# Kernel tuning notes

Hardware: AMD Instinct MI355X
Metric: run time of the kernel (lower is better)

Reference implementation:

```python
import jax, jax.numpy as jnp
import numpy as np

N, E, G = 100000, 1600000, 2048
F_NODE, F_EDGE, H, T = 32, 8, 128, 12


def _lin(key, fan_in, fan_out):
    k1, k2 = jax.random.split(key)
    s = 1.0 / np.sqrt(fan_in)
    W = jax.random.uniform(k1, (fan_in, fan_out), jnp.float32, -s, s)
    b = jax.random.uniform(k2, (fan_out,), jnp.float32, -s, s)
    return W, b


def setup_inputs() -> dict:
    key = jax.random.key(0)
    ks = jax.random.split(key, 12)
    x = jax.random.normal(ks[0], (N, F_NODE), jnp.float32)
    edge_index = jax.random.randint(ks[1], (2, E), 0, N, jnp.int64)
    edge_attr = jax.random.normal(ks[2], (E, F_EDGE), jnp.float32)
    batch = jnp.sort(jax.random.randint(ks[3], (N,), 0, G, jnp.int64))
    We1, be1 = _lin(ks[4], F_EDGE, F_NODE)   # conv1 edge lin: edge_dim -> in_channels
    W1a, b1a = _lin(ks[5], F_NODE, H)
    W1b, b1b = _lin(ks[6], H, H)
    We2, be2 = _lin(ks[7], F_EDGE, H)        # conv2 edge lin: edge_dim -> hidden
    W2a, b2a = _lin(ks[8], H, H)
    W2b, b2b = _lin(ks[9], H, H)
    Wl1, bl1 = _lin(ks[10], H, H)
    Wl2, bl2 = _lin(ks[11], H, T)
    return dict(x=x, edge_index=edge_index, edge_attr=edge_attr, batch=batch,
                We1=We1, be1=be1, W1a=W1a, b1a=b1a, W1b=W1b, b1b=b1b,
                We2=We2, be2=be2, W2a=W2a, b2a=b2a, W2b=W2b, b2b=b2b,
                Wl1=Wl1, bl1=bl1, Wl2=Wl2, bl2=bl2)


def _gine_conv(x, src, dst, edge_attr, We, be, Wa, ba, Wb, bb):
    # message: relu(x_j + Lin(edge_attr)), scatter-add to target, then MLP on (1+eps)*x + agg (eps=0)
    m = jax.nn.relu(x[src] + edge_attr @ We + be)          # [E, C]
    agg = jax.ops.segment_sum(m, dst, num_segments=x.shape[0])
    h = x + agg
    return jax.nn.elu(h @ Wa + ba) @ Wb + bb


def reference(x, edge_index, edge_attr, batch,
              We1, be1, W1a, b1a, W1b, b1b,
              We2, be2, W2a, b2a, W2b, b2b,
              Wl1, bl1, Wl2, bl2):
    src, dst = edge_index[0], edge_index[1]
    h = _gine_conv(x, src, dst, edge_attr, We1, be1, W1a, b1a, W1b, b1b)
    h = jax.nn.elu(h)  # dropout is identity at eval
    h = _gine_conv(h, src, dst, edge_attr, We2, be2, W2a, b2a, W2b, b2b)
    h = jax.nn.elu(h)
    hg = jax.ops.segment_sum(h, batch, num_segments=G)     # global add pool [G, H]
    hg = jax.nn.relu(hg @ Wl1 + bl1)
    return hg @ Wl2 + bl2                                  # [G, T]
```

## Files before the change

kernel.cpp:

```cpp
#include <hip/hip_runtime.h>
#include <math.h>

#define F_NODE 32
#define F_EDGE 8
#define HID 128
#define CAPB 6144

typedef __attribute__((ext_vector_type(2))) _Float16 f16x2;
typedef __attribute__((ext_vector_type(8))) _Float16 f16x8;
typedef __attribute__((ext_vector_type(4))) float f32x4;

__device__ __forceinline__ float elu_f(float x) { return x > 0.f ? x : expf(x) - 1.f; }

__device__ __forceinline__ unsigned h2u(f16x2 h) { union { f16x2 h; unsigned u; } x; x.h = h; return x.u; }
__device__ __forceinline__ f16x2 u2h(unsigned u) { union { unsigned u; f16x2 h; } x; x.u = u; return x.h; }
__device__ __forceinline__ unsigned packh2(float lo, float hi) {
    f16x2 v; v.x = (_Float16)lo; v.y = (_Float16)hi; return h2u(v);
}
__device__ __forceinline__ unsigned short f2h_bits(float f) {
    _Float16 h = (_Float16)f; union { _Float16 h; unsigned short u; } x; x.h = h; return x.u;
}
__device__ __forceinline__ f16x8 frag_from(uint4 v) { union { uint4 u; f16x8 f; } x; x.u = v; return x.f; }
__device__ __forceinline__ f16x2 duph(f16x8 v, int k) { f16x2 d; d.x = v[k]; d.y = v[k]; return d; }

__global__ void prep_kernel(const float* __restrict__ x, const float* __restrict__ ea,
                            const int* __restrict__ dst,
                            unsigned* __restrict__ xh, unsigned* __restrict__ eab,
                            const float* __restrict__ W1a, const float* __restrict__ W1b,
                            const float* __restrict__ W2a, const float* __restrict__ W2b,
                            const float* __restrict__ Wl1, const float* __restrict__ Wl2,
                            uint4* __restrict__ P1a, uint4* __restrict__ P1b,
                            uint4* __restrict__ P2a, uint4* __restrict__ P2b,
                            uint4* __restrict__ P3a, uint4* __restrict__ P3b,
                            int* __restrict__ cnt, int nx, int ne2, int E)
{
    int i = blockIdx.x * 256 + threadIdx.x;
    if (i < nx) {
        float2 v = ((const float2*)x)[i];
        xh[i] = packh2(v.x, v.y);
        return;
    }
    i -= nx;
    if (i < ne2) {
        float2 v = ((const float2*)ea)[i];
        eab[i] = packh2(v.x, v.y);
        return;
    }
    i -= ne2;
    if (i < 8960) {
        int f = i;
        if (f >= 8704) {
            f -= 8704;
            int lane = f & 63;
            int ks = f >> 6;
            int col = lane & 15;
            int k0 = ks * 32 + (lane >> 4) * 8;
            float w[8];
#pragma unroll
            for (int j = 0; j < 8; ++j) w[j] = col < 12 ? Wl2[(size_t)(k0 + j) * 12 + col] : 0.f;
            uint4 v;
            v.x = packh2(w[0], w[1]);
            v.y = packh2(w[2], w[3]);
            v.z = packh2(w[4], w[5]);
            v.w = packh2(w[6], w[7]);
            P3b[f] = v;
            return;
        }
        const float* W; uint4* P; int KS;
        if (f < 512)       { W = W1a; P = P1a; KS = 1; }
        else if (f < 2560) { W = W1b; P = P1b; KS = 4; f -= 512; }
        else if (f < 4608) { W = W2a; P = P2a; KS = 4; f -= 2560; }
        else if (f < 6656) { W = W2b; P = P2b; KS = 4; f -= 4608; }
        else               { W = Wl1; P = P3a; KS = 4; f -= 6656; }
        int lane = f & 63;
        int rem = f >> 6;
        int ks = rem % KS, ct = rem / KS;
        int col = ct * 16 + (lane & 15);
        int k0 = ks * 32 + (lane >> 4) * 8;
        float w[8];
#pragma unroll
        for (int j = 0; j < 8; ++j) w[j] = W[(size_t)(k0 + j) * HID + col];
        uint4 v;
        v.x = packh2(w[0], w[1]);
        v.y = packh2(w[2], w[3]);
        v.z = packh2(w[4], w[5]);
        v.w = packh2(w[6], w[7]);
        P[f] = v;
        return;
    }
    i -= 8960;
    if (i < E) atomicAdd(&cnt[dst[i]], 1);
}

__global__ void scan1_kernel(const int* __restrict__ in, int* __restrict__ out,
                             int* __restrict__ part, int n) {
    __shared__ int s[256];
    int t = threadIdx.x;
    int base = blockIdx.x * 1024 + t * 4;
    int v0 = base + 0 < n ? in[base + 0] : 0;
    int v1 = base + 1 < n ? in[base + 1] : 0;
    int v2 = base + 2 < n ? in[base + 2] : 0;
    int v3 = base + 3 < n ? in[base + 3] : 0;
    int tot = v0 + v1 + v2 + v3;
    s[t] = tot;
    __syncthreads();
    for (int off = 1; off < 256; off <<= 1) {
        int val = (t >= off) ? s[t - off] : 0;
        __syncthreads();
        s[t] += val;
        __syncthreads();
    }
    int pre = s[t] - tot;
    if (base + 0 < n) out[base + 0] = pre;
    if (base + 1 < n) out[base + 1] = pre + v0;
    if (base + 2 < n) out[base + 2] = pre + v0 + v1;
    if (base + 3 < n) out[base + 3] = pre + v0 + v1 + v2;
    if (t == 255) part[blockIdx.x] = s[255];
}

__global__ void scan2_kernel(int* part, int nb) {
    __shared__ int s[256];
    int t = threadIdx.x;
    int v = t < nb ? part[t] : 0;
    s[t] = v;
    __syncthreads();
    for (int off = 1; off < 256; off <<= 1) {
        int val = (t >= off) ? s[t - off] : 0;
        __syncthreads();
        s[t] += val;
        __syncthreads();
    }
    if (t < nb) part[t] = s[t] - v;
}

__global__ void scan3_kernel(int* __restrict__ out, const int* __restrict__ part,
                             int* __restrict__ curB, int* __restrict__ curFine,
                             int n, int total) {
    int i = blockIdx.x * blockDim.x + threadIdx.x;
    if (i < n) {
        int v = out[i] + part[i >> 10];
        out[i] = v;
        curFine[i] = v;
        if ((i & 255) == 0) curB[i >> 8] = v;
    }
    if (i == 0) out[n] = total;
}

__global__ __launch_bounds__(256) void binA_kernel(
    const int* __restrict__ dst, const int* __restrict__ src,
    int* __restrict__ curB, int2* __restrict__ tmp, int E, int NB)
{
    __shared__ int hist[512];
    __shared__ int basev[512];
    const int tid = threadIdx.x;
    const int base = blockIdx.x * 4096;
    for (int i = tid; i < NB; i += 256) hist[i] = 0;
    __syncthreads();
    int d[16];
#pragma unroll
    for (int k = 0; k < 16; ++k) {
        int e = base + k * 256 + tid;
        d[k] = (e < E) ? dst[e] : -1;
        if (d[k] >= 0) atomicAdd(&hist[d[k] >> 8], 1);
    }
    __syncthreads();
    for (int i = tid; i < NB; i += 256) {
        int c = hist[i];
        basev[i] = c > 0 ? atomicAdd(&curB[i], c) : 0;
        hist[i] = 0;
    }
    __syncthreads();
#pragma unroll
    for (int k = 0; k < 16; ++k) {
        int e = base + k * 256 + tid;
        if (d[k] >= 0) {
            int b = d[k] >> 8;
            int r = atomicAdd(&hist[b], 1);
            tmp[basev[b] + r] = make_int2(e | ((d[k] & 255) << 22), src[e]);
        }
    }
}

__global__ __launch_bounds__(256) void binB_kernel(
    const int2* __restrict__ tmp, const int* __restrict__ off,
    int* __restrict__ curFine, int2* __restrict__ pair, int N)
{
    __shared__ int ldsCur[256];
    __shared__ int2 stage[CAPB];
    const int b = blockIdx.x;
    const int tid = threadIdx.x;
    const int node0 = b << 8;
    const int nend = min(node0 + 256, N);
    const int base = off[node0];
    const int end = off[nend];
    const int S = end - base;
    if (S <= CAPB) {
        int node = node0 + tid;
        ldsCur[tid] = (node < nend ? off[node] : end) - base;
        __syncthreads();
        for (int j = tid; j < S; j += 256) {
            int2 rec = tmp[base + j];
            int dloc = ((unsigned)rec.x) >> 22;
            int slot = atomicAdd(&ldsCur[dloc], 1);
            stage[slot] = make_int2(rec.x & 0x3FFFFF, rec.y);
        }
        __syncthreads();
        for (int j = tid; j < S; j += 256)
            pair[base + j] = stage[j];
    } else {
        for (int j = tid; j < S; j += 256) {
            int2 rec = tmp[base + j];
            int dloc = ((unsigned)rec.x) >> 22;
            int pos = atomicAdd(&curFine[node0 + dloc], 1);
            pair[pos] = make_int2(rec.x & 0x3FFFFF, rec.y);
        }
    }
}

__global__ __launch_bounds__(256) void agg1_kernel(
    const float* __restrict__ x, const unsigned* __restrict__ xh,
    const uint4* __restrict__ eab4,
    const float* __restrict__ We, const float* __restrict__ be,
    const int* __restrict__ off, const int2* __restrict__ pair,
    unsigned* __restrict__ aggh, int N)
{
    int wave = (blockIdx.x * 256 + threadIdx.x) >> 6;
    if (wave >= N) return;
    int lane = threadIdx.x & 63;
    int fp = lane & 15, eg = lane >> 4;
    int j0 = fp * 2;
    f16x2 w2[F_EDGE];
#pragma unroll
    for (int k = 0; k < F_EDGE; ++k)
        w2[k] = u2h(packh2(We[k * F_NODE + j0], We[k * F_NODE + j0 + 1]));
    f16x2 bias2 = u2h(packh2(be[j0], be[j0 + 1]));
    f16x2 zero2 = u2h(0u);
    int i0 = __builtin_amdgcn_readfirstlane(off[wave]);
    int i1 = __builtin_amdgcn_readfirstlane(off[wave + 1]);
    float acc0 = 0.f, acc1 = 0.f;
    for (int i = i0; i < i1; i += 4) {
        int ii = i + eg;
        if (ii < i1) {
            int2 p = pair[ii];
            f16x8 ev = frag_from(eab4[p.x]);
            f16x2 m = bias2 + u2h(xh[(size_t)p.y * 16 + fp]);
#pragma unroll
            for (int k = 0; k < F_EDGE; ++k)
                m = duph(ev, k) * w2[k] + m;
            m = __builtin_elementwise_max(m, zero2);
            acc0 += (float)m.x;
            acc1 += (float)m.y;
        }
    }
    acc0 += __shfl_xor(acc0, 16, 64);
    acc0 += __shfl_xor(acc0, 32, 64);
    acc1 += __shfl_xor(acc1, 16, 64);
    acc1 += __shfl_xor(acc1, 32, 64);
    if (eg == 0) {
        float2 xo = *(const float2*)&x[(size_t)wave * F_NODE + j0];
        aggh[(size_t)wave * 16 + fp] = packh2(xo.x + acc0, xo.y + acc1);
    }
}

__global__ __launch_bounds__(256) void agg2_kernel(
    const unsigned* __restrict__ hh,
    const uint4* __restrict__ eab4,
    const float* __restrict__ We, const float* __restrict__ be,
    const int* __restrict__ off, const int2* __restrict__ pair,
    unsigned* __restrict__ aggh, int N)
{
    int wave = (blockIdx.x * 256 + threadIdx.x) >> 6;
    if (wave >= N) return;
    int lane = threadIdx.x & 63;
    int j0 = lane * 2;
    f16x2 w2[F_EDGE];
#pragma unroll
    for (int k = 0; k < F_EDGE; ++k)
        w2[k] = u2h(packh2(We[k * HID + j0], We[k * HID + j0 + 1]));
    f16x2 bias2 = u2h(packh2(be[j0], be[j0 + 1]));
    f16x2 zero2 = u2h(0u);
    int i0 = __builtin_amdgcn_readfirstlane(off[wave]);
    int i1 = __builtin_amdgcn_readfirstlane(off[wave + 1]);
    float acc0 = 0.f, acc1 = 0.f;
    int i = i0;
    for (; i + 7 < i1; i += 8) {
        int2 p[8];
        unsigned u[8];
        f16x8 ev[8];
#pragma unroll
        for (int k = 0; k < 8; ++k) p[k] = pair[i + k];
#pragma unroll
        for (int k = 0; k < 8; ++k) u[k] = hh[(size_t)p[k].y * 64 + lane];
#pragma unroll
        for (int k = 0; k < 8; ++k) ev[k] = frag_from(eab4[p[k].x]);
        f16x2 m[8];
#pragma unroll
        for (int k = 0; k < 8; ++k) m[k] = bias2 + u2h(u[k]);
#pragma unroll
        for (int kk = 0; kk < F_EDGE; ++kk) {
#pragma unroll
            for (int k = 0; k < 8; ++k)
                m[k] = duph(ev[k], kk) * w2[kk] + m[k];
        }
        f16x2 s = __builtin_elementwise_max(m[0], zero2);
#pragma unroll
        for (int k = 1; k < 8; ++k) s = s + __builtin_elementwise_max(m[k], zero2);
        acc0 += (float)s.x;
        acc1 += (float)s.y;
    }
    for (; i < i1; ++i) {
        int2 p0 = pair[i];
        f16x8 e0 = frag_from(eab4[p0.x]);
        f16x2 m0 = bias2 + u2h(hh[(size_t)p0.y * 64 + lane]);
#pragma unroll
        for (int k = 0; k < F_EDGE; ++k)
            m0 = duph(e0, k) * w2[k] + m0;
        m0 = __builtin_elementwise_max(m0, zero2);
        acc0 += (float)m0.x;
        acc1 += (float)m0.y;
    }
    f16x2 self = u2h(hh[(size_t)wave * 64 + lane]);
    aggh[(size_t)wave * 64 + lane] = packh2((float)self.x + acc0, (float)self.y + acc1);
}

__device__ __forceinline__ void put_tile_elu_h(unsigned short* t, f32x4 v, int rbase, int c, int stride) {
#pragma unroll
    for (int j = 0; j < 4; ++j)
        t[(rbase + j) * stride + c] = f2h_bits(elu_f(v[j]));
}
__device__ __forceinline__ void put_tile_relu_h(unsigned short* t, f32x4 v, int rbase, int c, int stride) {
#pragma unroll
    for (int j = 0; j < 4; ++j)
        t[(rbase + j) * stride + c] = f2h_bits(fmaxf(v[j], 0.f));
}

template <int K, bool POOL>
__global__ __launch_bounds__(256) void mlp_mfma_kernel(
    const uint4* __restrict__ inb,
    const uint4* __restrict__ WaP, const float* __restrict__ ba,
    const uint4* __restrict__ WbP, const float* __restrict__ bb,
    uint4* __restrict__ outb,
    const int* __restrict__ batch, float* __restrict__ hg,
    int nrows)
{
    constexpr int KS_A = K / 32;
    constexpr int SA = K + 8;
    constexpr int ST = HID + 8;
    constexpr int STF = HID + 4;
    __shared__ __align__(16) unsigned short a_s[32 * SA];
    __shared__ __align__(16) unsigned short t_s[32 * ST];
    __shared__ float p_s[POOL ? 32 * STF : 1];
    __shared__ int batch_s[POOL ? 32 : 1];

    const int tid = threadIdx.x;
    const int row0 = blockIdx.x * 32;

    constexpr int Q = K / 8;
    for (int idx = tid; idx < 32 * Q; idx += 256) {
        int r = idx / Q, q = idx % Q;
        uint4 v = make_uint4(0, 0, 0, 0);
        if (row0 + r < nrows) v = inb[(size_t)(row0 + r) * Q + q];
        *(uint4*)&a_s[r * SA + q * 8] = v;
    }
    if (POOL && tid < 32)
        batch_s[tid] = (row0 + tid < nrows) ? batch[row0 + tid] : -1;
    __syncthreads();

    const int lane = tid & 63;
    const int w = tid >> 6;
    const int rb = w >> 1;
    const int cg = (w & 1) * 4;
    const int cf = lane & 15;
    const int g = lane >> 4;
    const int arow = rb * 16 + cf;

    f32x4 acc0, acc1, acc2, acc3;
    {
        float c0 = ba[(cg + 0) * 16 + cf], c1 = ba[(cg + 1) * 16 + cf];
        float c2 = ba[(cg + 2) * 16 + cf], c3 = ba[(cg + 3) * 16 + cf];
        acc0 = (f32x4){c0, c0, c0, c0};
        acc1 = (f32x4){c1, c1, c1, c1};
        acc2 = (f32x4){c2, c2, c2, c2};
        acc3 = (f32x4){c3, c3, c3, c3};
    }
#pragma unroll
    for (int ks = 0; ks < KS_A; ++ks) {
        f16x8 a = *(const f16x8*)&a_s[arow * SA + ks * 32 + g * 8];
        acc0 = __builtin_amdgcn_mfma_f32_16x16x32_f16(a, frag_from(WaP[((cg + 0) * KS_A + ks) * 64 + lane]), acc0, 0, 0, 0);
        acc1 = __builtin_amdgcn_mfma_f32_16x16x32_f16(a, frag_from(WaP[((cg + 1) * KS_A + ks) * 64 + lane]), acc1, 0, 0, 0);
        acc2 = __builtin_amdgcn_mfma_f32_16x16x32_f16(a, frag_from(WaP[((cg + 2) * KS_A + ks) * 64 + lane]), acc2, 0, 0, 0);
        acc3 = __builtin_amdgcn_mfma_f32_16x16x32_f16(a, frag_from(WaP[((cg + 3) * KS_A + ks) * 64 + lane]), acc3, 0, 0, 0);
    }
    {
        int rbase = rb * 16 + g * 4;
        put_tile_elu_h(t_s, acc0, rbase, (cg + 0) * 16 + cf, ST);
        put_tile_elu_h(t_s, acc1, rbase, (cg + 1) * 16 + cf, ST);
        put_tile_elu_h(t_s, acc2, rbase, (cg + 2) * 16 + cf, ST);
        put_tile_elu_h(t_s, acc3, rbase, (cg + 3) * 16 + cf, ST);
    }
    __syncthreads();

    {
        float c0 = bb[(cg + 0) * 16 + cf], c1 = bb[(cg + 1) * 16 + cf];
        float c2 = bb[(cg + 2) * 16 + cf], c3 = bb[(cg + 3) * 16 + cf];
        acc0 = (f32x4){c0, c0, c0, c0};
        acc1 = (f32x4){c1, c1, c1, c1};
        acc2 = (f32x4){c2, c2, c2, c2};
        acc3 = (f32x4){c3, c3, c3, c3};
    }
#pragma unroll
    for (int ks = 0; ks < 4; ++ks) {
        f16x8 a = *(const f16x8*)&t_s[arow * ST + ks * 32 + g * 8];
        acc0 = __builtin_amdgcn_mfma_f32_16x16x32_f16(a, frag_from(WbP[((cg + 0) * 4 + ks) * 64 + lane]), acc0, 0, 0, 0);
        acc1 = __builtin_amdgcn_mfma_f32_16x16x32_f16(a, frag_from(WbP[((cg + 1) * 4 + ks) * 64 + lane]), acc1, 0, 0, 0);
        acc2 = __builtin_amdgcn_mfma_f32_16x16x32_f16(a, frag_from(WbP[((cg + 2) * 4 + ks) * 64 + lane]), acc2, 0, 0, 0);
        acc3 = __builtin_amdgcn_mfma_f32_16x16x32_f16(a, frag_from(WbP[((cg + 3) * 4 + ks) * 64 + lane]), acc3, 0, 0, 0);
    }

    if (POOL) {
        int rbase = rb * 16 + g * 4;
#pragma unroll
        for (int j = 0; j < 4; ++j) {
            p_s[(rbase + j) * STF + (cg + 0) * 16 + cf] = elu_f(acc0[j]);
            p_s[(rbase + j) * STF + (cg + 1) * 16 + cf] = elu_f(acc1[j]);
            p_s[(rbase + j) * STF + (cg + 2) * 16 + cf] = elu_f(acc2[j]);
            p_s[(rbase + j) * STF + (cg + 3) * 16 + cf] = elu_f(acc3[j]);
        }
        __syncthreads();
        int f = tid & 127, grp = tid >> 7;
        float acc = 0.f;
        int cur = -1;
#pragma unroll 4
        for (int r = 0; r < 16; ++r) {
            int rr = grp * 16 + r;
            int b = batch_s[rr];
            if (b >= 0) {
                if (b != cur) {
                    if (cur >= 0) atomicAdd(&hg[(size_t)cur * HID + f], acc);
                    acc = 0.f;
                    cur = b;
                }
                acc += p_s[rr * STF + f];
            }
        }
        if (cur >= 0) atomicAdd(&hg[(size_t)cur * HID + f], acc);
    } else {
        __syncthreads();
        int rbase = rb * 16 + g * 4;
        put_tile_elu_h(t_s, acc0, rbase, (cg + 0) * 16 + cf, ST);
        put_tile_elu_h(t_s, acc1, rbase, (cg + 1) * 16 + cf, ST);
        put_tile_elu_h(t_s, acc2, rbase, (cg + 2) * 16 + cf, ST);
        put_tile_elu_h(t_s, acc3, rbase, (cg + 3) * 16 + cf, ST);
        __syncthreads();
        for (int idx = tid; idx < 32 * 16; idx += 256) {
            int r = idx >> 4, q = idx & 15;
            if (row0 + r < nrows)
                outb[(size_t)(row0 + r) * 16 + q] = *(const uint4*)&t_s[r * ST + q * 8];
        }
    }
}

__global__ __launch_bounds__(256) void head_mfma_kernel(
    const float* __restrict__ hg,
    const uint4* __restrict__ Wl1P, const float* __restrict__ bl1,
    const uint4* __restrict__ Wl2P, const float* __restrict__ bl2,
    float* __restrict__ out, int G)
{
    constexpr int ST = HID + 8;
    __shared__ __align__(16) unsigned short a_s[32 * ST];
    __shared__ __align__(16) unsigned short t_s[32 * ST];

    const int tid = threadIdx.x;
    const int row0 = blockIdx.x * 32;

    for (int idx = tid; idx < 32 * HID; idx += 256) {
        int r = idx >> 7, c = idx & 127;
        float v = (row0 + r < G) ? hg[(size_t)(row0 + r) * HID + c] : 0.f;
        a_s[r * ST + c] = f2h_bits(v);
    }
    __syncthreads();

    const int lane = tid & 63;
    const int w = tid >> 6;
    const int rb = w >> 1;
    const int cg = (w & 1) * 4;
    const int cf = lane & 15;
    const int g = lane >> 4;
    const int arow = rb * 16 + cf;

    f32x4 acc0, acc1, acc2, acc3;
    {
        float c0 = bl1[(cg + 0) * 16 + cf], c1 = bl1[(cg + 1) * 16 + cf];
        float c2 = bl1[(cg + 2) * 16 + cf], c3 = bl1[(cg + 3) * 16 + cf];
        acc0 = (f32x4){c0, c0, c0, c0};
        acc1 = (f32x4){c1, c1, c1, c1};
        acc2 = (f32x4){c2, c2, c2, c2};
        acc3 = (f32x4){c3, c3, c3, c3};
    }
#pragma unroll
    for (int ks = 0; ks < 4; ++ks) {
        f16x8 a = *(const f16x8*)&a_s[arow * ST + ks * 32 + g * 8];
        acc0 = __builtin_amdgcn_mfma_f32_16x16x32_f16(a, frag_from(Wl1P[((cg + 0) * 4 + ks) * 64 + lane]), acc0, 0, 0, 0);
        acc1 = __builtin_amdgcn_mfma_f32_16x16x32_f16(a, frag_from(Wl1P[((cg + 1) * 4 + ks) * 64 + lane]), acc1, 0, 0, 0);
        acc2 = __builtin_amdgcn_mfma_f32_16x16x32_f16(a, frag_from(Wl1P[((cg + 2) * 4 + ks) * 64 + lane]), acc2, 0, 0, 0);
        acc3 = __builtin_amdgcn_mfma_f32_16x16x32_f16(a, frag_from(Wl1P[((cg + 3) * 4 + ks) * 64 + lane]), acc3, 0, 0, 0);
    }
    {
        int rbase = rb * 16 + g * 4;
        put_tile_relu_h(t_s, acc0, rbase, (cg + 0) * 16 + cf, ST);
        put_tile_relu_h(t_s, acc1, rbase, (cg + 1) * 16 + cf, ST);
        put_tile_relu_h(t_s, acc2, rbase, (cg + 2) * 16 + cf, ST);
        put_tile_relu_h(t_s, acc3, rbase, (cg + 3) * 16 + cf, ST);
    }
    __syncthreads();

    if ((w & 1) == 0) {
        float c0 = cf < 12 ? bl2[cf] : 0.f;
        f32x4 acc = (f32x4){c0, c0, c0, c0};
#pragma unroll
        for (int ks = 0; ks < 4; ++ks) {
            f16x8 a = *(const f16x8*)&t_s[arow * ST + ks * 32 + g * 8];
            acc = __builtin_amdgcn_mfma_f32_16x16x32_f16(a, frag_from(Wl2P[ks * 64 + lane]), acc, 0, 0, 0);
        }
        if (cf < 12) {
            int rbase = rb * 16 + g * 4;
#pragma unroll
            for (int j = 0; j < 4; ++j) {
                int row = row0 + rbase + j;
                if (row < G) out[(size_t)row * 12 + cf] = acc[j];
            }
        }
    }
}

extern "C" void kernel_launch(void* const* d_in, const int* in_sizes, int n_in,
                              void* d_out, int out_size, void* d_ws, size_t ws_size,
                              hipStream_t stream)
{
    const float* x    = (const float*)d_in[0];
    const int*   ei   = (const int*)d_in[1];
    const float* ea   = (const float*)d_in[2];
    const int*   batch = (const int*)d_in[3];
    const float* We1 = (const float*)d_in[4];
    const float* be1 = (const float*)d_in[5];
    const float* W1a = (const float*)d_in[6];
    const float* b1a = (const float*)d_in[7];
    const float* W1b = (const float*)d_in[8];
    const float* b1b = (const float*)d_in[9];
    const float* We2 = (const float*)d_in[10];
    const float* be2 = (const float*)d_in[11];
    const float* W2a = (const float*)d_in[12];
    const float* b2a = (const float*)d_in[13];
    const float* W2b = (const float*)d_in[14];
    const float* b2b = (const float*)d_in[15];
    const float* Wl1 = (const float*)d_in[16];
    const float* bl1 = (const float*)d_in[17];
    const float* Wl2 = (const float*)d_in[18];
    const float* bl2 = (const float*)d_in[19];
    float* out = (float*)d_out;

    const int N = in_sizes[0] / F_NODE;
    const int E = in_sizes[1] / 2;
    const int G = out_size / 12;
    const int NB = (N + 255) >> 8;

    const int* srcp = ei;
    const int* dstp = ei + E;

    char* wsb = (char*)d_ws;
    auto alloc = [&](size_t bytes) -> char* {
        char* p = wsb;
        wsb += (bytes + 15) & ~(size_t)15;
        return p;
    };
    int* cnt     = (int*)alloc((size_t)N * 4);
    int* off     = (int*)alloc((size_t)(N + 1) * 4);
    int* part    = (int*)alloc(256 * 4);
    int* curB    = (int*)alloc(512 * 4);
    int* curFine = (int*)alloc((size_t)N * 4);
    int2* tmp    = (int2*)alloc((size_t)E * 8);
    int2* pair   = (int2*)alloc((size_t)E * 8);
    unsigned* xh   = (unsigned*)alloc((size_t)N * 16 * 4);
    unsigned* eab  = (unsigned*)alloc((size_t)E * 4 * 4);
    unsigned* agg1h = (unsigned*)alloc((size_t)N * 16 * 4);
    unsigned* h1h   = (unsigned*)alloc((size_t)N * 64 * 4);
    unsigned* agg2h = (unsigned*)alloc((size_t)N * 64 * 4);
    float* hg  = (float*)alloc((size_t)G * HID * 4);
    uint4* P1a = (uint4*)alloc(512 * 16);
    uint4* P1b = (uint4*)alloc(2048 * 16);
    uint4* P2a = (uint4*)alloc(2048 * 16);
    uint4* P2b = (uint4*)alloc(2048 * 16);
    uint4* P3a = (uint4*)alloc(2048 * 16);
    uint4* P3b = (uint4*)alloc(256 * 16);

    (void)hipMemsetAsync(cnt, 0, (size_t)N * sizeof(int), stream);
    (void)hipMemsetAsync(hg, 0, (size_t)G * HID * sizeof(float), stream);

    {
        int nx = N * 16, ne2 = E * 4;
        long long total = (long long)nx + ne2 + 8960 + E;
        hipLaunchKernelGGL(prep_kernel, dim3((unsigned)((total + 255) / 256)), dim3(256), 0, stream,
                           x, ea, dstp, xh, eab, W1a, W1b, W2a, W2b, Wl1, Wl2,
                           P1a, P1b, P2a, P2b, P3a, P3b, cnt, nx, ne2, E);
    }
    int nscan = (N + 1023) / 1024;
    hipLaunchKernelGGL(scan1_kernel, dim3(nscan), dim3(256), 0, stream, cnt, off, part, N);
    hipLaunchKernelGGL(scan2_kernel, dim3(1), dim3(256), 0, stream, part, nscan);
    hipLaunchKernelGGL(scan3_kernel, dim3((N + 255) / 256), dim3(256), 0, stream,
                       off, part, curB, curFine, N, E);
    hipLaunchKernelGGL(binA_kernel, dim3((E + 4095) / 4096), dim3(256), 0, stream,
                       dstp, srcp, curB, tmp, E, NB);
    hipLaunchKernelGGL(binB_kernel, dim3(NB), dim3(256), 0, stream,
                       tmp, off, curFine, pair, N);

    hipLaunchKernelGGL(agg1_kernel, dim3((N + 3) / 4), dim3(256), 0, stream,
                       x, xh, (const uint4*)eab, We1, be1, off, pair, agg1h, N);
    hipLaunchKernelGGL((mlp_mfma_kernel<F_NODE, false>), dim3((N + 31) / 32), dim3(256), 0, stream,
                       (const uint4*)agg1h, P1a, b1a, P1b, b1b, (uint4*)h1h,
                       (const int*)nullptr, (float*)nullptr, N);

    hipLaunchKernelGGL(agg2_kernel, dim3((N + 3) / 4), dim3(256), 0, stream,
                       h1h, (const uint4*)eab, We2, be2, off, pair, agg2h, N);
    hipLaunchKernelGGL((mlp_mfma_kernel<HID, true>), dim3((N + 31) / 32), dim3(256), 0, stream,
                       (const uint4*)agg2h, P2a, b2a, P2b, b2b, (uint4*)nullptr,
                       batch, hg, N);

    hipLaunchKernelGGL(head_mfma_kernel, dim3((G + 31) / 32), dim3(256), 0, stream,
                       hg, P3a, bl1, P3b, bl2, out, G);
}
```

Before: 375.3 us.

## Pre-sort edge attributes by destination and gather FP8 hidden features in conv2

binB now writes a source array plus a copy of each edge's attribute vector in destination-sorted order. Both aggregation kernels can then stream edge features contiguously instead of gathering them by edge id. The first MLP also writes an FP8 copy of the hidden features, which agg2 gathers at half the bytes per neighbor compared with FP16. This cuts random-access traffic in the dominant gather at the cost of lower precision for layer-2 messages, an extra sorted-copy write, and buffer aliasing (h8 reuses tmp, agg2h reuses eab).

After: 368.5 us. No clear change (-1.8%).

```diff
diff --git a/kernel.cpp b/kernel.cpp
--- a/kernel.cpp
+++ b/kernel.cpp
@@ -9,6 +9,7 @@
 typedef __attribute__((ext_vector_type(2))) _Float16 f16x2;
 typedef __attribute__((ext_vector_type(8))) _Float16 f16x8;
 typedef __attribute__((ext_vector_type(4))) float f32x4;
+typedef __attribute__((ext_vector_type(2))) float f32x2;
 
 __device__ __forceinline__ float elu_f(float x) { return x > 0.f ? x : expf(x) - 1.f; }
 
@@ -19,6 +20,9 @@
 }
 __device__ __forceinline__ unsigned short f2h_bits(float f) {
     _Float16 h = (_Float16)f; union { _Float16 h; unsigned short u; } x; x.h = h; return x.u;
+}
+__device__ __forceinline__ float hbits2f(unsigned short b) {
+    union { unsigned short u; _Float16 h; } x; x.u = b; return (float)x.h;
 }
 __device__ __forceinline__ f16x8 frag_from(uint4 v) { union { uint4 u; f16x8 f; } x; x.u = v; return x.f; }
 __device__ __forceinline__ f16x2 duph(f16x8 v, int k) { f16x2 d; d.x = v[k]; d.y = v[k]; return d; }
@@ -183,7 +187,8 @@
 
 __global__ __launch_bounds__(256) void binB_kernel(
     const int2* __restrict__ tmp, const int* __restrict__ off,
-    int* __restrict__ curFine, int2* __restrict__ pair, int N)
+    int* __restrict__ curFine, const uint4* __restrict__ eab4,
+    int* __restrict__ srcarr, uint4* __restrict__ easrt, int N)
 {
     __shared__ int ldsCur[256];
     __shared__ int2 stage[CAPB];
@@ -205,23 +210,28 @@
             stage[slot] = make_int2(rec.x & 0x3FFFFF, rec.y);
         }
         __syncthreads();
-        for (int j = tid; j < S; j += 256)
-            pair[base + j] = stage[j];
+        for (int j = tid; j < S; j += 256) {
+            int2 rec = stage[j];
+            srcarr[base + j] = rec.y;
+            easrt[base + j] = eab4[rec.x];
+        }
     } else {
         for (int j = tid; j < S; j += 256) {
             int2 rec = tmp[base + j];
             int dloc = ((unsigned)rec.x) >> 22;
+            int e = rec.x & 0x3FFFFF;
             int pos = atomicAdd(&curFine[node0 + dloc], 1);
-            pair[pos] = make_int2(rec.x & 0x3FFFFF, rec.y);
+            srcarr[pos] = rec.y;
+            easrt[pos] = eab4[e];
         }
     }
 }
 
 __global__ __launch_bounds__(256) void agg1_kernel(
     const float* __restrict__ x, const unsigned* __restrict__ xh,
-    const uint4* __restrict__ eab4,
+    const uint4* __restrict__ easrt,
     const float* __restrict__ We, const float* __restrict__ be,
-    const int* __restrict__ off, const int2* __restrict__ pair,
+    const int* __restrict__ off, const int* __restrict__ srcarr,
     unsigned* __restrict__ aggh, int N)
 {
     int wave = (blockIdx.x * 256 + threadIdx.x) >> 6;
@@ -241,9 +251,9 @@
     for (int i = i0; i < i1; i += 4) {
         int ii = i + eg;
         if (ii < i1) {
-            int2 p = pair[ii];
-            f16x8 ev = frag_from(eab4[p.x]);
-            f16x2 m = bias2 + u2h(xh[(size_t)p.y * 16 + fp]);
+            int s = srcarr[ii];
+            f16x8 ev = frag_from(easrt[ii]);
+            f16x2 m = bias2 + u2h(xh[(size_t)s * 16 + fp]);
 #pragma unroll
             for (int k = 0; k < F_EDGE; ++k)
                 m = duph(ev, k) * w2[k] + m;
@@ -263,10 +273,10 @@
 }
 
 __global__ __launch_bounds__(256) void agg2_kernel(
-    const unsigned* __restrict__ hh,
-    const uint4* __restrict__ eab4,
+    const unsigned* __restrict__ hh, const unsigned short* __restrict__ h8,
+    const uint4* __restrict__ easrt,
     const float* __restrict__ We, const float* __restrict__ be,
-    const int* __restrict__ off, const int2* __restrict__ pair,
+    const int* __restrict__ off, const int* __restrict__ srcarr,
     unsigned* __restrict__ aggh, int N)
 {
     int wave = (blockIdx.x * 256 + threadIdx.x) >> 6;
@@ -284,34 +294,40 @@
     float acc0 = 0.f, acc1 = 0.f;
     int i = i0;
     for (; i + 7 < i1; i += 8) {
-        int2 p[8];
-        unsigned u[8];
+        int s[8];
+        unsigned short u[8];
         f16x8 ev[8];
 #pragma unroll
-        for (int k = 0; k < 8; ++k) p[k] = pair[i + k];
-#pragma unroll
-        for (int k = 0; k < 8; ++k) u[k] = hh[(size_t)p[k].y * 64 + lane];
-#pragma unroll
-        for (int k = 0; k < 8; ++k) ev[k] = frag_from(eab4[p[k].x]);
+        for (int k = 0; k < 8; ++k) s[k] = srcarr[i + k];
+#pragma unroll
+        for (int k = 0; k < 8; ++k) u[k] = h8[(size_t)s[k] * 64 + lane];
+#pragma unroll
+        for (int k = 0; k < 8; ++k) ev[k] = frag_from(easrt[i + k]);
         f16x2 m[8];
 #pragma unroll
-        for (int k = 0; k < 8; ++k) m[k] = bias2 + u2h(u[k]);
+        for (int k = 0; k < 8; ++k) {
+            f32x2 f = __builtin_amdgcn_cvt_pk_f32_fp8((int)u[k], false);
+            f16x2 hv; hv.x = (_Float16)f.x; hv.y = (_Float16)f.y;
+            m[k] = bias2 + hv;
+        }
 #pragma unroll
         for (int kk = 0; kk < F_EDGE; ++kk) {
 #pragma unroll
             for (int k = 0; k < 8; ++k)
                 m[k] = duph(ev[k], kk) * w2[kk] + m[k];
         }
-        f16x2 s = __builtin_elementwise_max(m[0], zero2);
-#pragma unroll
-        for (int k = 1; k < 8; ++k) s = s + __builtin_elementwise_max(m[k], zero2);
-        acc0 += (float)s.x;
-        acc1 += (float)s.y;
+        f16x2 sm = __builtin_elementwise_max(m[0], zero2);
+#pragma unroll
+        for (int k = 1; k < 8; ++k) sm = sm + __builtin_elementwise_max(m[k], zero2);
+        acc0 += (float)sm.x;
+        acc1 += (float)sm.y;
     }
     for (; i < i1; ++i) {
-        int2 p0 = pair[i];
-        f16x8 e0 = frag_from(eab4[p0.x]);
-        f16x2 m0 = bias2 + u2h(hh[(size_t)p0.y * 64 + lane]);
+        int s0 = srcarr[i];
+        f16x8 e0 = frag_from(easrt[i]);
+        f32x2 f = __builtin_amdgcn_cvt_pk_f32_fp8((int)h8[(size_t)s0 * 64 + lane], false);
+        f16x2 hv; hv.x = (_Float16)f.x; hv.y = (_Float16)f.y;
+        f16x2 m0 = bias2 + hv;
 #pragma unroll
         for (int k = 0; k < F_EDGE; ++k)
             m0 = duph(e0, k) * w2[k] + m0;
@@ -334,12 +350,12 @@
         t[(rbase + j) * stride + c] = f2h_bits(fmaxf(v[j], 0.f));
 }
 
-template <int K, bool POOL>
+template <int K, bool POOL, bool DUP8>
 __global__ __launch_bounds__(256) void mlp_mfma_kernel(
     const uint4* __restrict__ inb,
     const uint4* __restrict__ WaP, const float* __restrict__ ba,
     const uint4* __restrict__ WbP, const float* __restrict__ bb,
-    uint4* __restrict__ outb,
+    uint4* __restrict__ outb, unsigned* __restrict__ out8,
     const int* __restrict__ batch, float* __restrict__ hg,
     int nrows)
 {
@@ -456,6 +472,20 @@
             int r = idx >> 4, q = idx & 15;
             if (row0 + r < nrows)
                 outb[(size_t)(row0 + r) * 16 + q] = *(const uint4*)&t_s[r * ST + q * 8];
+        }
+        if (DUP8) {
+            for (int idx = tid; idx < 32 * 32; idx += 256) {
+                int r = idx >> 5, q = idx & 31;
+                if (row0 + r < nrows) {
+                    float f0 = hbits2f(t_s[r * ST + q * 4 + 0]);
+                    float f1 = hbits2f(t_s[r * ST + q * 4 + 1]);
+                    float f2 = hbits2f(t_s[r * ST + q * 4 + 2]);
+                    float f3 = hbits2f(t_s[r * ST + q * 4 + 3]);
+                    int u = __builtin_amdgcn_cvt_pk_fp8_f32(f0, f1, 0, false);
+                    u = __builtin_amdgcn_cvt_pk_fp8_f32(f2, f3, u, true);
+                    out8[(size_t)(row0 + r) * 32 + q] = (unsigned)u;
+                }
+            }
         }
     }
 }
@@ -579,12 +609,14 @@
     int* curB    = (int*)alloc(512 * 4);
     int* curFine = (int*)alloc((size_t)N * 4);
     int2* tmp    = (int2*)alloc((size_t)E * 8);
-    int2* pair   = (int2*)alloc((size_t)E * 8);
+    unsigned short* h8 = (unsigned short*)tmp;
+    int* srcarr  = (int*)alloc((size_t)E * 4);
+    uint4* easrt = (uint4*)alloc((size_t)E * 16);
     unsigned* xh   = (unsigned*)alloc((size_t)N * 16 * 4);
     unsigned* eab  = (unsigned*)alloc((size_t)E * 4 * 4);
+    unsigned* agg2h = eab;
     unsigned* agg1h = (unsigned*)alloc((size_t)N * 16 * 4);
     unsigned* h1h   = (unsigned*)alloc((size_t)N * 64 * 4);
-    unsigned* agg2h = (unsigned*)alloc((size_t)N * 64 * 4);
     float* hg  = (float*)alloc((size_t)G * HID * 4);
     uint4* P1a = (uint4*)alloc(512 * 16);
     uint4* P1b = (uint4*)alloc(2048 * 16);
@@ -611,18 +643,18 @@
     hipLaunchKernelGGL(binA_kernel, dim3((E + 4095) / 4096), dim3(256), 0, stream,
                        dstp, srcp, curB, tmp, E, NB);
     hipLaunchKernelGGL(binB_kernel, dim3(NB), dim3(256), 0, stream,
-                       tmp, off, curFine, pair, N);
+                       tmp, off, curFine, (const uint4*)eab, srcarr, easrt, N);
 
     hipLaunchKernelGGL(agg1_kernel, dim3((N + 3) / 4), dim3(256), 0, stream,
-                       x, xh, (const uint4*)eab, We1, be1, off, pair, agg1h, N);
-    hipLaunchKernelGGL((mlp_mfma_kernel<F_NODE, false>), dim3((N + 31) / 32), dim3(256), 0, stream,
-                       (const uint4*)agg1h, P1a, b1a, P1b, b1b, (uint4*)h1h,
+                       x, xh, easrt, We1, be1, off, srcarr, agg1h, N);
+    hipLaunchKernelGGL((mlp_mfma_kernel<F_NODE, false, true>), dim3((N + 31) / 32), dim3(256), 0, stream,
+                       (const uint4*)agg1h, P1a, b1a, P1b, b1b, (uint4*)h1h, (unsigned*)h8,
                        (const int*)nullptr, (float*)nullptr, N);
 
     hipLaunchKernelGGL(agg2_kernel, dim3((N + 3) / 4), dim3(256), 0, stream,
-                       h1h, (const uint4*)eab, We2, be2, off, pair, agg2h, N);
-    hipLaunchKernelGGL((mlp_mfma_kernel<HID, true>), dim3((N + 31) / 32), dim3(256), 0, stream,
-                       (const uint4*)agg2h, P2a, b2a, P2b, b2b, (uint4*)nullptr,
+                       h1h, h8, easrt, We2, be2, off, srcarr, agg2h, N);
+    hipLaunchKernelGGL((mlp_mfma_kernel<HID, true, false>), dim3((N + 31) / 32), dim3(256), 0, stream,
+                       (const uint4*)agg2h, P2a, b2a, P2b, b2b, (uint4*)nullptr, (unsigned*)nullptr,
                        batch, hg, N);
 
     hipLaunchKernelGGL(head_mfma_kernel, dim3((G + 31) / 32), dim3(256), 0, stream,
```
